# Kernel tuning notes

Hardware: AMD Instinct MI355X
Metric: run time of the kernel (lower is better)

## Reference

```python
import jax, jax.numpy as jnp
import numpy as np

B, N, E = 32, 2000, 32000      # graphs, nodes/graph, edges/graph
V, D, R, K = 100000, 128, 39, 8  # vocab, emb_dim, n_relation, n_bases
EPS = 1e-5


def setup_inputs() -> dict:
    key = jax.random.key(0)
    ks = jax.random.split(key, 8)
    node_ids = jax.random.randint(ks[0], (B, N), 0, V)
    edge_index = jax.random.randint(ks[1], (B, 2, E), 0, N)
    edge_type = jax.random.randint(ks[2], (B, E), 0, R)
    embedding = jax.random.normal(ks[3], (V, D), jnp.float32) * D ** -0.5
    bases = jax.random.normal(ks[4], (K, D, D), jnp.float32) * D ** -0.5
    comp = jax.random.normal(ks[5], (R, K), jnp.float32) * K ** -0.5
    root = jax.random.normal(ks[6], (D, D), jnp.float32) * D ** -0.5
    bias = jnp.zeros((D,), jnp.float32)
    return dict(node_ids=node_ids, edge_index=edge_index, edge_type=edge_type,
                embedding=embedding, bases=bases, comp=comp, root=root, bias=bias)


def _graph_fwd(node_ids, edge_index, edge_type, embedding, bases, comp, root, bias):
    # RGCNConv with basis decomposition and per-relation MEAN aggregation (PyG default).
    x = embedding[node_ids]                       # [N, D] per-graph node features
    src, dst = edge_index[0], edge_index[1]       # j -> i, aggregate at dst
    x_src = x[src]                                # [E, D]
    # mean normalizer per (dst, relation) bucket
    comb = dst * R + edge_type                    # [E]
    cnt = jax.ops.segment_sum(jnp.ones((E,), jnp.float32), comb, num_segments=N * R)
    inv = jnp.where(cnt > 0, 1.0 / cnt, 0.0)[comb]  # [E]
    # W_r = sum_k comp[r,k] * bases[k]; fold comp coefficients + mean norm into edge weights
    w = comp[edge_type] * inv[:, None]            # [E, K]
    out = x @ root + bias                         # root/self connection
    for k in range(K):                            # small fixed loop over bases
        zk = jax.ops.segment_sum(w[:, k:k + 1] * x_src, dst, num_segments=N)  # [N, D]
        out = out + zk @ bases[k]
    g = out.sum(axis=0)                           # sum pool over nodes
    # torch.nn.functional.normalize(p=2, eps=1e-5)
    return g / jnp.maximum(jnp.linalg.norm(g), EPS)


def reference(node_ids, edge_index, edge_type, embedding, bases, comp, root, bias):
    f = jax.vmap(_graph_fwd, in_axes=(0, 0, 0, None, None, None, None, None))
    return f(node_ids, edge_index, edge_type, embedding, bases, comp, root, bias)  # [B, D]
```

## Files before the change

kernel.cpp:

```cpp
#include <hip/hip_runtime.h>
#include <math.h>

#define Bn 32
#define Nn 2000
#define En 32000
#define Vn 100000
#define Dn 128
#define Rn 39
#define Kn 8

#define SUBS 8
#define NPS (Nn / SUBS)
#define NPAIR (Nn / 2)
#define EQ (En / 4)
#define NR (NPS * Rn)
#define NRS 78080
#define GBLK 16
#define WSLOT (GBLK * 8)


__global__ __launch_bounds__(1024) void count_kernel(const int* __restrict__ edge_index,
                                                     const int* __restrict__ edge_type,
                                                     unsigned char* __restrict__ cntg) {
    int b = blockIdx.x, sub = blockIdx.y;
    int base = sub * NR;
    __shared__ int loc[NR];
    for (int i = threadIdx.x; i < NR; i += 1024) loc[i] = 0;
    __syncthreads();
    const int4* dst4 = (const int4*)(edge_index + (b * 2 + 1) * En);
    const int4* et4  = (const int4*)(edge_type + b * En);
    for (int q = threadIdx.x; q < EQ; q += 1024) {
        int4 d = dst4[q]; int4 t = et4[q]; int y;
        y = d.x * Rn + t.x - base; if ((unsigned)y < NR) atomicAdd(&loc[y], 1);
        y = d.y * Rn + t.y - base; if ((unsigned)y < NR) atomicAdd(&loc[y], 1);
        y = d.z * Rn + t.z - base; if ((unsigned)y < NR) atomicAdd(&loc[y], 1);
        y = d.w * Rn + t.w - base; if ((unsigned)y < NR) atomicAdd(&loc[y], 1);
    }
    __syncthreads();
    unsigned char* cg = cntg + (size_t)b * NRS + base;
    for (int i = threadIdx.x; i < NR; i += 1024) {
        int c = loc[i];
        cg[i] = (unsigned char)(c > 255 ? 255 : c);
    }
}

__global__ __launch_bounds__(1024) void a_kernel(const int* __restrict__ edge_index,
                                                 const int* __restrict__ edge_type,
                                                 const unsigned char* __restrict__ cntg,
                                                 const float* __restrict__ comp,
                                                 float* __restrict__ a) {
    int b = blockIdx.x, sub = blockIdx.y;
    int base = sub * NR;
    __shared__ float s[NR];
    __shared__ float comp_l[Rn * Kn];
    for (int i = threadIdx.x; i < NR; i += 1024) s[i] = 0.0f;
    if (threadIdx.x < Rn * Kn) comp_l[threadIdx.x] = comp[threadIdx.x];
    __syncthreads();
    const int4* src4 = (const int4*)(edge_index + (b * 2 + 0) * En);
    const int4* dst4 = (const int4*)(edge_index + (b * 2 + 1) * En);
    const int4* et4  = (const int4*)(edge_type + b * En);
    const unsigned char* cg = cntg + (size_t)b * NRS;
    for (int q = threadIdx.x; q < EQ; q += 1024) {
        int4 sv = src4[q]; int4 dv = dst4[q]; int4 tv = et4[q]; int y;
        y = sv.x * Rn + tv.x - base;
        if ((unsigned)y < NR) atomicAdd(&s[y], 1.0f / (float)cg[dv.x * Rn + tv.x]);
        y = sv.y * Rn + tv.y - base;
        if ((unsigned)y < NR) atomicAdd(&s[y], 1.0f / (float)cg[dv.y * Rn + tv.y]);
        y = sv.z * Rn + tv.z - base;
        if ((unsigned)y < NR) atomicAdd(&s[y], 1.0f / (float)cg[dv.z * Rn + tv.z]);
        y = sv.w * Rn + tv.w - base;
        if ((unsigned)y < NR) atomicAdd(&s[y], 1.0f / (float)cg[dv.w * Rn + tv.w]);
    }
    __syncthreads();
    float* g = a + ((size_t)b * Nn + sub * NPS) * Kn;
    for (int i = threadIdx.x; i < NPS * Kn; i += 1024) {
        int n = i >> 3, k = i & 7;
        float acc = 0.0f;
        const float* srow = &s[n * Rn];
        for (int t = 0; t < Rn; t++) acc += srow[t] * comp_l[t * Kn + k];
        g[i] = acc;
    }
}

__global__ __launch_bounds__(512, 4) void gather_kernel(const int* __restrict__ node_ids,
                                                        const float* __restrict__ emb,
                                                        const float* __restrict__ a,
                                                        float* __restrict__ partial) {
    int b = blockIdx.x;
    int lane = threadIdx.x & 63, wv = threadIdx.x >> 6;
    int Wl = blockIdx.y * 8 + wv;
    int half = lane >> 5;
    int dl = lane & 31;
    __shared__ float red[8][9][Dn];
    float4 acc[9];
#pragma unroll
    for (int k = 0; k < 9; k++) acc[k] = make_float4(0.f, 0.f, 0.f, 0.f);
    const int*   nb = node_ids + b * Nn;
    const float* ab = a + (size_t)b * Nn * Kn;
#pragma unroll
    for (int i0 = 0; i0 < 8; i0 += 4) {
        bool   has[4];
        int    node[4];
        float4 v[4];
        float4 a0[4], a1[4];
#pragma unroll
        for (int i = 0; i < 4; i++) {
            int p = Wl + (i0 + i) * WSLOT;
            has[i] = p < NPAIR;
            node[i] = (has[i] ? 2 * p : 0) + half;
        }
#pragma unroll
        for (int i = 0; i < 4; i++) {
            int nid = nb[node[i]];
            v[i] = has[i] ? ((const float4*)(emb + (size_t)nid * Dn))[dl]
                          : make_float4(0.f, 0.f, 0.f, 0.f);
            const float4* ar = (const float4*)(ab + (size_t)node[i] * Kn);
            a0[i] = ar[0]; a1[i] = ar[1];
        }
#pragma unroll
        for (int i = 0; i < 4; i++) {
            float w[9] = {a0[i].x, a0[i].y, a0[i].z, a0[i].w,
                          a1[i].x, a1[i].y, a1[i].z, a1[i].w, 1.0f};
#pragma unroll
            for (int k = 0; k < 9; k++) {
                acc[k].x += w[k] * v[i].x;
                acc[k].y += w[k] * v[i].y;
                acc[k].z += w[k] * v[i].z;
                acc[k].w += w[k] * v[i].w;
            }
        }
    }
#pragma unroll
    for (int k = 0; k < 9; k++) {
        acc[k].x += __shfl_down(acc[k].x, 32, 64);
        acc[k].y += __shfl_down(acc[k].y, 32, 64);
        acc[k].z += __shfl_down(acc[k].z, 32, 64);
        acc[k].w += __shfl_down(acc[k].w, 32, 64);
    }
    if (half == 0) {
#pragma unroll
        for (int k = 0; k < 9; k++)
            ((float4*)red[wv][k])[dl] = acc[k];
    }
    __syncthreads();
    int slot = threadIdx.x;
    if (slot < 9 * (Dn / 4)) {
        int k = slot >> 5, d4 = slot & 31;
        float4 t = make_float4(0.f, 0.f, 0.f, 0.f);
#pragma unroll
        for (int w = 0; w < 8; w++) {
            float4 v = ((const float4*)red[w][k])[d4];
            t.x += v.x; t.y += v.y; t.z += v.z; t.w += v.w;
        }
        float4* gp = (float4*)(partial + (((size_t)b * 9 + k) * GBLK + blockIdx.y) * Dn);
        gp[d4] = t;
    }
}

__global__ __launch_bounds__(256) void matvec_kernel(const float* __restrict__ partial,
                                                     const float* __restrict__ root,
                                                     const float* __restrict__ bases,
                                                     float* __restrict__ gmat) {
    int b = blockIdx.x, m = blockIdx.y;
    int tid = threadIdx.x;
    __shared__ float4 ts4[Dn / 4];
    __shared__ float tsh[8][Dn];
    int dg = tid & 31, part = tid >> 5;
    const float4* p4 = (const float4*)(partial + ((size_t)b * 9 + m) * GBLK * Dn);
    float4 sum = make_float4(0.f, 0.f, 0.f, 0.f);
    for (int c = part; c < GBLK; c += 8) {
        float4 v = p4[c * 32 + dg];
        sum.x += v.x; sum.y += v.y; sum.z += v.z; sum.w += v.w;
    }
    ((float4*)tsh[part])[dg] = sum;
    __syncthreads();
    if (part == 0) {
        float4 t = make_float4(0.f, 0.f, 0.f, 0.f);
#pragma unroll
        for (int r = 0; r < 8; r++) {
            float4 v = ((float4*)tsh[r])[dg];
            t.x += v.x; t.y += v.y; t.z += v.z; t.w += v.w;
        }
        ts4[dg] = t;
    }
    __syncthreads();
    const float* ts = (const float*)ts4;
    const float* M  = (m == 8) ? root : bases + (size_t)m * Dn * Dn;
    int d = tid & (Dn - 1), h = tid >> 7;
    float g = 0.0f;
#pragma unroll 8
    for (int j = h * 64; j < h * 64 + 64; j++) g += ts[j] * M[j * Dn + d];
    __syncthreads();
    tsh[h][d] = g;
    __syncthreads();
    if (h == 0) gmat[((size_t)b * 9 + m) * Dn + d] = tsh[0][d] + tsh[1][d];
}

__global__ __launch_bounds__(128) void norm_kernel(const float* __restrict__ gmat,
                                                   const float* __restrict__ bias,
                                                   float* __restrict__ out) {
    int b = blockIdx.x, d = threadIdx.x;
    float g = (float)Nn * bias[d];
    const float* gb = gmat + (size_t)b * 9 * Dn + d;
#pragma unroll
    for (int m = 0; m < 9; m++) g += gb[m * Dn];
    float ss = g * g;
#pragma unroll
    for (int off = 32; off > 0; off >>= 1) ss += __shfl_down(ss, off, 64);
    __shared__ float s2[2];
    if ((threadIdx.x & 63) == 0) s2[threadIdx.x >> 6] = ss;
    __syncthreads();
    float nrm = sqrtf(s2[0] + s2[1]);
    out[b * Dn + d] = g / fmaxf(nrm, 1e-5f);
}

extern "C" void kernel_launch(void* const* d_in, const int* in_sizes, int n_in,
                              void* d_out, int out_size, void* d_ws, size_t ws_size,
                              hipStream_t stream) {
    const int*   node_ids   = (const int*)d_in[0];
    const int*   edge_index = (const int*)d_in[1];
    const int*   edge_type  = (const int*)d_in[2];
    const float* embedding  = (const float*)d_in[3];
    const float* bases      = (const float*)d_in[4];
    const float* comp       = (const float*)d_in[5];
    const float* root       = (const float*)d_in[6];
    const float* bias       = (const float*)d_in[7];
    float*       out        = (float*)d_out;

    char* w = (char*)d_ws;
    unsigned char* cntg    = (unsigned char*)(w + 0);
    float*         a       = (float*)(w + 2498560);
    float*         partial = (float*)(w + 4546560);
    float*         gmat    = (float*)(w + 6905856);

    count_kernel <<<dim3(Bn, SUBS), 1024, 0, stream>>>(edge_index, edge_type, cntg);
    a_kernel     <<<dim3(Bn, SUBS), 1024, 0, stream>>>(edge_index, edge_type, cntg, comp, a);
    gather_kernel<<<dim3(Bn, GBLK), 512,  0, stream>>>(node_ids, embedding, a, partial);
    matvec_kernel<<<dim3(Bn, 9),    256,  0, stream>>>(partial, root, bases, gmat);
    norm_kernel  <<<Bn, 128, 0, stream>>>(gmat, bias, out);
}
```

Measured before the change: 142.1 us.

## Stage count table in LDS with reciprocal LUT and fuse matvec with normalization

The a_kernel now copies the graph's whole byte count table (78 KB) into shared memory and looks up reciprocals in a 256-entry table. This replaces scattered global byte loads and per-edge divisions. The matvec and norm kernels become a single finish kernel, one block per graph, which removes a launch and the gmat round trip. In exchange the larger LDS footprint lowers a_kernel occupancy, and the fused kernel runs only 32 blocks that each do nine 128x128 matvecs serially.

Measured after the change: 144.9 us. No clear change (+2.0%).

```diff
diff --git a/kernel.cpp b/kernel.cpp
--- a/kernel.cpp
+++ b/kernel.cpp
@@ -14,6 +14,7 @@
 #define NPAIR (Nn / 2)
 #define EQ (En / 4)
 #define NR (NPS * Rn)
+#define NRT (Nn * Rn)
 #define NRS 78080
 #define GBLK 16
 #define WSLOT (GBLK * 8)
@@ -52,24 +53,31 @@
     int b = blockIdx.x, sub = blockIdx.y;
     int base = sub * NR;
     __shared__ float s[NR];
+    __shared__ unsigned char cnt_l[NRT] __attribute__((aligned(16)));
+    __shared__ float lut[256];
     __shared__ float comp_l[Rn * Kn];
     for (int i = threadIdx.x; i < NR; i += 1024) s[i] = 0.0f;
+    {
+        const int4* src = (const int4*)(cntg + (size_t)b * NRS);
+        int4* dst = (int4*)cnt_l;
+        for (int i = threadIdx.x; i < NRT / 16; i += 1024) dst[i] = src[i];
+    }
+    if (threadIdx.x < 256) lut[threadIdx.x] = 1.0f / (float)threadIdx.x;
     if (threadIdx.x < Rn * Kn) comp_l[threadIdx.x] = comp[threadIdx.x];
     __syncthreads();
     const int4* src4 = (const int4*)(edge_index + (b * 2 + 0) * En);
     const int4* dst4 = (const int4*)(edge_index + (b * 2 + 1) * En);
     const int4* et4  = (const int4*)(edge_type + b * En);
-    const unsigned char* cg = cntg + (size_t)b * NRS;
     for (int q = threadIdx.x; q < EQ; q += 1024) {
         int4 sv = src4[q]; int4 dv = dst4[q]; int4 tv = et4[q]; int y;
         y = sv.x * Rn + tv.x - base;
-        if ((unsigned)y < NR) atomicAdd(&s[y], 1.0f / (float)cg[dv.x * Rn + tv.x]);
+        if ((unsigned)y < NR) atomicAdd(&s[y], lut[cnt_l[dv.x * Rn + tv.x]]);
         y = sv.y * Rn + tv.y - base;
-        if ((unsigned)y < NR) atomicAdd(&s[y], 1.0f / (float)cg[dv.y * Rn + tv.y]);
+        if ((unsigned)y < NR) atomicAdd(&s[y], lut[cnt_l[dv.y * Rn + tv.y]]);
         y = sv.z * Rn + tv.z - base;
-        if ((unsigned)y < NR) atomicAdd(&s[y], 1.0f / (float)cg[dv.z * Rn + tv.z]);
+        if ((unsigned)y < NR) atomicAdd(&s[y], lut[cnt_l[dv.z * Rn + tv.z]]);
         y = sv.w * Rn + tv.w - base;
-        if ((unsigned)y < NR) atomicAdd(&s[y], 1.0f / (float)cg[dv.w * Rn + tv.w]);
+        if ((unsigned)y < NR) atomicAdd(&s[y], lut[cnt_l[dv.w * Rn + tv.w]]);
     }
     __syncthreads();
     float* g = a + ((size_t)b * Nn + sub * NPS) * Kn;
@@ -157,61 +165,53 @@
     }
 }
 
-__global__ __launch_bounds__(256) void matvec_kernel(const float* __restrict__ partial,
+__global__ __launch_bounds__(512) void finish_kernel(const float* __restrict__ partial,
                                                      const float* __restrict__ root,
                                                      const float* __restrict__ bases,
-                                                     float* __restrict__ gmat) {
-    int b = blockIdx.x, m = blockIdx.y;
-    int tid = threadIdx.x;
-    __shared__ float4 ts4[Dn / 4];
-    __shared__ float tsh[8][Dn];
-    int dg = tid & 31, part = tid >> 5;
-    const float4* p4 = (const float4*)(partial + ((size_t)b * 9 + m) * GBLK * Dn);
-    float4 sum = make_float4(0.f, 0.f, 0.f, 0.f);
-    for (int c = part; c < GBLK; c += 8) {
-        float4 v = p4[c * 32 + dg];
-        sum.x += v.x; sum.y += v.y; sum.z += v.z; sum.w += v.w;
-    }
-    ((float4*)tsh[part])[dg] = sum;
-    __syncthreads();
-    if (part == 0) {
-        float4 t = make_float4(0.f, 0.f, 0.f, 0.f);
-#pragma unroll
-        for (int r = 0; r < 8; r++) {
-            float4 v = ((float4*)tsh[r])[dg];
-            t.x += v.x; t.y += v.y; t.z += v.z; t.w += v.w;
-        }
-        ts4[dg] = t;
-    }
-    __syncthreads();
-    const float* ts = (const float*)ts4;
-    const float* M  = (m == 8) ? root : bases + (size_t)m * Dn * Dn;
-    int d = tid & (Dn - 1), h = tid >> 7;
-    float g = 0.0f;
-#pragma unroll 8
-    for (int j = h * 64; j < h * 64 + 64; j++) g += ts[j] * M[j * Dn + d];
-    __syncthreads();
-    tsh[h][d] = g;
-    __syncthreads();
-    if (h == 0) gmat[((size_t)b * 9 + m) * Dn + d] = tsh[0][d] + tsh[1][d];
-}
-
-__global__ __launch_bounds__(128) void norm_kernel(const float* __restrict__ gmat,
-                                                   const float* __restrict__ bias,
-                                                   float* __restrict__ out) {
-    int b = blockIdx.x, d = threadIdx.x;
+                                                     const float* __restrict__ bias,
+                                                     float* __restrict__ out) {
+    int b = blockIdx.x, tid = threadIdx.x;
+    __shared__ float ts[9][Dn];
+    __shared__ float4 red4[16][Dn / 4];
+    __shared__ float ssr[8];
+    for (int slot = tid; slot < 9 * Dn; slot += 512) {
+        int k = slot >> 7, d = slot & 127;
+        const float* pp = partial + (((size_t)b * 9 + k) * GBLK) * Dn + d;
+        float t = 0.0f;
+#pragma unroll
+        for (int c = 0; c < GBLK; c++) t += pp[c * Dn];
+        ts[k][d] = t;
+    }
+    __syncthreads();
+    int d4 = tid & 31, jg = tid >> 5;
+    float4 acc = make_float4(0.f, 0.f, 0.f, 0.f);
+    for (int m = 0; m < 9; m++) {
+        const float4* M4 = (const float4*)((m == 8) ? root : bases + (size_t)m * Dn * Dn);
+        const float* tsm = ts[m];
+#pragma unroll
+        for (int jj = 0; jj < 8; jj++) {
+            int j = jg * 8 + jj;
+            float w = tsm[j];
+            float4 mv = M4[j * 32 + d4];
+            acc.x += w * mv.x; acc.y += w * mv.y; acc.z += w * mv.z; acc.w += w * mv.w;
+        }
+    }
+    red4[jg][d4] = acc;
+    __syncthreads();
+    const float* redf = (const float*)red4;
+    int d = tid & 127;
     float g = (float)Nn * bias[d];
-    const float* gb = gmat + (size_t)b * 9 * Dn + d;
-#pragma unroll
-    for (int m = 0; m < 9; m++) g += gb[m * Dn];
+#pragma unroll
+    for (int w = 0; w < 16; w++) g += redf[w * Dn + d];
     float ss = g * g;
 #pragma unroll
     for (int off = 32; off > 0; off >>= 1) ss += __shfl_down(ss, off, 64);
-    __shared__ float s2[2];
-    if ((threadIdx.x & 63) == 0) s2[threadIdx.x >> 6] = ss;
-    __syncthreads();
-    float nrm = sqrtf(s2[0] + s2[1]);
-    out[b * Dn + d] = g / fmaxf(nrm, 1e-5f);
+    if ((tid & 63) == 0) ssr[tid >> 6] = ss;
+    __syncthreads();
+    float tot = (ssr[0] + ssr[1] + ssr[2] + ssr[3] +
+                 ssr[4] + ssr[5] + ssr[6] + ssr[7]) * 0.25f;
+    float nrm = sqrtf(tot);
+    if (tid < Dn) out[b * Dn + tid] = g / fmaxf(nrm, 1e-5f);
 }
 
 extern "C" void kernel_launch(void* const* d_in, const int* in_sizes, int n_in,
@@ -231,11 +231,9 @@
     unsigned char* cntg    = (unsigned char*)(w + 0);
     float*         a       = (float*)(w + 2498560);
     float*         partial = (float*)(w + 4546560);
-    float*         gmat    = (float*)(w + 6905856);
 
     count_kernel <<<dim3(Bn, SUBS), 1024, 0, stream>>>(edge_index, edge_type, cntg);
     a_kernel     <<<dim3(Bn, SUBS), 1024, 0, stream>>>(edge_index, edge_type, cntg, comp, a);
     gather_kernel<<<dim3(Bn, GBLK), 512,  0, stream>>>(node_ids, embedding, a, partial);
-    matvec_kernel<<<dim3(Bn, 9),    256,  0, stream>>>(partial, root, bases, gmat);
-    norm_kernel  <<<Bn, 128, 0, stream>>>(gmat, bias, out);
-}
+    finish_kernel<<<Bn, 512, 0, stream>>>(partial, root, bases, bias, out);
+}
```
